# Kernel tuning notes

Measured on AMD Instinct MI355X. Metric: run time of the kernel, lower is better.

## Reference

```python
import jax, jax.numpy as jnp
import numpy as np
from jax import lax
import math

D_MODEL = 768
EXPAND = 2
D_INNER = EXPAND * D_MODEL          # 1536 (= d_ssm since d_ssm=None)
D_STATE = 128
HEADDIM = 64
NHEADS = D_INNER // HEADDIM         # 24
D_CONV = 4
NGROUPS = 1
CONV_DIM = D_INNER + 2 * NGROUPS * D_STATE            # 1792
D_IN_PROJ = 2 * D_INNER + 2 * NGROUPS * D_STATE + NHEADS  # d_mlp = 0
BATCH, SEQLEN = 2, 2048
EPS = 1e-5


def setup_inputs() -> dict:
    key = jax.random.key(0)
    ks = jax.random.split(key, 8)
    u = jax.random.normal(ks[0], (BATCH, SEQLEN, D_MODEL), dtype=jnp.float32)
    in_proj_w = jax.random.normal(ks[1], (D_IN_PROJ, D_MODEL), dtype=jnp.float32) / math.sqrt(D_MODEL)
    conv_w = jax.random.uniform(ks[2], (CONV_DIM, D_CONV), dtype=jnp.float32, minval=-0.5, maxval=0.5)
    conv_b = jnp.zeros((CONV_DIM,), dtype=jnp.float32)
    # dt_bias = inverse-softplus of dt sampled log-uniform in [1e-3, 1e-1]
    dt = jnp.exp(jax.random.uniform(ks[3], (NHEADS,)) * (math.log(0.1) - math.log(0.001)) + math.log(0.001))
    dt_bias = dt + jnp.log(-jnp.expm1(-dt))
    A_log = jnp.log(jax.random.uniform(ks[4], (NHEADS,), minval=1.0, maxval=16.0))
    D = jnp.ones((NHEADS,), dtype=jnp.float32)
    norm_w = jnp.ones((D_INNER,), dtype=jnp.float32)
    out_proj_w = jax.random.normal(ks[5], (D_MODEL, D_INNER), dtype=jnp.float32) / math.sqrt(D_INNER)
    return {"u": u, "in_proj_w": in_proj_w, "conv_w": conv_w, "conv_b": conv_b,
            "dt_bias": dt_bias, "A_log": A_log, "D": D, "norm_w": norm_w,
            "out_proj_w": out_proj_w}


def _mamba2_forward(u, in_proj_w, conv_w, conv_b, dt_bias, A_log, D, norm_w, out_proj_w):
    b, l, _ = u.shape
    zxbcdt = u @ in_proj_w.T                                   # [b,l,D_IN_PROJ]
    z = zxbcdt[..., :D_INNER]                                  # [b,l,d_ssm]
    xBC = zxbcdt[..., D_INNER:D_INNER + CONV_DIM]              # [b,l,conv_dim]
    dt = zxbcdt[..., D_INNER + CONV_DIM:]                      # [b,l,h]

    # causal depthwise conv1d (pad d_conv-1 left == torch pad both + truncate tail)
    xBC_t = xBC.transpose(0, 2, 1)                             # [b,c,l]
    conv_out = lax.conv_general_dilated(
        xBC_t, conv_w[:, None, :], window_strides=(1,),
        padding=[(D_CONV - 1, 0)], feature_group_count=CONV_DIM,
        dimension_numbers=("NCH", "OIH", "NCH"))
    xBC = jax.nn.silu(conv_out + conv_b[None, :, None]).transpose(0, 2, 1)  # [b,l,c]

    x = xBC[..., :D_INNER].reshape(b, l, NHEADS, HEADDIM)      # [b,l,h,p]
    B = xBC[..., D_INNER:D_INNER + D_STATE]                    # [b,l,n]
    C = xBC[..., D_INNER + D_STATE:]                           # [b,l,n]

    A = -jnp.exp(A_log)                                        # [h]
    dt_dis = jax.nn.softplus(dt + dt_bias)                     # [b,l,h]  (dt_limit=(0,inf) -> no-op clamp)
    dA = jnp.exp(dt_dis * A)                                   # [b,l,h]

    def step(state, inp):
        dA_t, dt_t, B_t, x_t, C_t = inp
        dBx = jnp.einsum("bh,bn,bhp->bhpn", dt_t, B_t, x_t)    # [b,h,p,n]
        state = lax.stop_gradient(state * dA_t[:, :, None, None] + dBx)  # matches torch .detach()
        y_t = jnp.einsum("bhpn,bn->bhp", state, C_t)
        return state, y_t

    xs = (dA.transpose(1, 0, 2), dt_dis.transpose(1, 0, 2),
          B.transpose(1, 0, 2), x.transpose(1, 0, 2, 3), C.transpose(1, 0, 2))
    state0 = jnp.zeros((b, NHEADS, HEADDIM, D_STATE), dtype=u.dtype)
    _, ys = lax.scan(step, state0, xs)                         # [l,b,h,p]
    y = ys.transpose(1, 0, 2, 3) + x * D[None, None, :, None]  # D skip (per-head)
    y = y.reshape(b, l, D_INNER)

    # gated RMSNorm (norm_before_gate=False, group_size = d_ssm)
    yz = y * jax.nn.silu(z)
    y = yz * lax.rsqrt(jnp.mean(yz * yz, axis=-1, keepdims=True) + EPS) * norm_w

    return y @ out_proj_w.T                                    # [b,l,d_model]


def reference(u, in_proj_w, conv_w, conv_b, dt_bias, A_log, D, norm_w, out_proj_w):
    return _mamba2_forward(u, in_proj_w, conv_w, conv_b, dt_bias, A_log, D, norm_w, out_proj_w)
```

## Files before the change

kernel.cpp:

```cpp
#include <hip/hip_runtime.h>
#include <hip/hip_bf16.h>
#include <math.h>

#define D_MODEL   768
#define D_INNER   1536
#define D_STATE   128
#define HEADDIM   64
#define NHEADS    24
#define D_CONV    4
#define CONV_DIM  1792
#define D_IN_PROJ 3352
#define BATCH     2
#define SEQLEN    2048
#define NROWS     (BATCH*SEQLEN)
#define EPS       1e-5f

#define NCHUNK    16
#define CHUNK     128
#define STATE_SZ  (HEADDIM*D_STATE)

#define N1_PAD    3456
#define LDST      136
#define H72       72

typedef __bf16 bf16x8 __attribute__((ext_vector_type(8)));
typedef float  f32x4  __attribute__((ext_vector_type(4)));

__device__ __forceinline__ short f2b(float f) {
    unsigned u = __float_as_uint(f);
    unsigned r = (u + 0x7FFFu + ((u >> 16) & 1u)) >> 16;
    return (short)r;
}

__global__ __launch_bounds__(256) void gemm_bf16_kernel(
    const short* __restrict__ A, const short* __restrict__ W,
    float* __restrict__ C, int K, int Nreal)
{
    __shared__ short As[128][32];
    __shared__ short Bs[128][32];
    const int m0 = blockIdx.y * 128;
    const int n0 = blockIdx.x * 128;
    const int tid  = threadIdx.x;
    const int lane = tid & 63;
    const int wid  = tid >> 6;
    const int wm = wid >> 1, wn = wid & 1;
    const int lr = lane & 15;
    const int kg = lane >> 4;

    f32x4 acc[4][4];
    #pragma unroll
    for (int i = 0; i < 4; ++i)
        #pragma unroll
        for (int j = 0; j < 4; ++j)
            acc[i][j] = (f32x4){0.f, 0.f, 0.f, 0.f};

    const int srow = (lane >> 2);
    const int scol = (lane & 3) * 8;

    for (int k0 = 0; k0 < K; k0 += 32) {
        #pragma unroll
        for (int it = 0; it < 2; ++it) {
            int r = wid * 32 + it * 16 + srow;
            const short* ga = A + (size_t)(m0 + r) * K + k0 + scol;
            const short* gw = W + (size_t)(n0 + r) * K + k0 + scol;
            __builtin_amdgcn_global_load_lds(
                (const __attribute__((address_space(1))) void*)ga,
                (__attribute__((address_space(3))) void*)&As[wid * 32 + it * 16][0],
                16, 0, 0);
            __builtin_amdgcn_global_load_lds(
                (const __attribute__((address_space(1))) void*)gw,
                (__attribute__((address_space(3))) void*)&Bs[wid * 32 + it * 16][0],
                16, 0, 0);
        }
        __syncthreads();

        bf16x8 af[4], bf[4];
        #pragma unroll
        for (int i = 0; i < 4; ++i)
            af[i] = *(const bf16x8*)&As[wm * 64 + i * 16 + lr][kg * 8];
        #pragma unroll
        for (int j = 0; j < 4; ++j)
            bf[j] = *(const bf16x8*)&Bs[wn * 64 + j * 16 + lr][kg * 8];
        #pragma unroll
        for (int i = 0; i < 4; ++i)
            #pragma unroll
            for (int j = 0; j < 4; ++j)
                acc[i][j] = __builtin_amdgcn_mfma_f32_16x16x32_bf16(af[i], bf[j], acc[i][j], 0, 0, 0);
        __syncthreads();
    }

    #pragma unroll
    for (int i = 0; i < 4; ++i) {
        int mrow = m0 + wm * 64 + i * 16 + kg * 4;
        #pragma unroll
        for (int j = 0; j < 4; ++j) {
            int ncol = n0 + wn * 64 + j * 16 + lr;
            if (ncol < Nreal) {
                #pragma unroll
                for (int r = 0; r < 4; ++r)
                    C[(size_t)(mrow + r) * Nreal + ncol] = acc[i][j][r];
            }
        }
    }
}

__global__ __launch_bounds__(256) void cast_bf16_kernel(
    const float* __restrict__ in, short* __restrict__ out, int n4)
{
    int i = blockIdx.x * 256 + threadIdx.x;
    if (i >= n4) return;
    float4 v = *(const float4*)(in + (size_t)i * 4);
    short4 o = make_short4(f2b(v.x), f2b(v.y), f2b(v.z), f2b(v.w));
    *(short4*)(out + (size_t)i * 4) = o;
}

__global__ __launch_bounds__(256) void cast_pad_w1_kernel(
    const float* __restrict__ w, short* __restrict__ wb)
{
    int i = blockIdx.x * 256 + threadIdx.x;
    const int n4 = N1_PAD * D_MODEL / 4;
    if (i >= n4) return;
    size_t base = (size_t)i * 4;
    int row = (int)(base / D_MODEL);
    float4 v = make_float4(0.f, 0.f, 0.f, 0.f);
    if (row < D_IN_PROJ) v = *(const float4*)(w + base);
    short4 o = make_short4(f2b(v.x), f2b(v.y), f2b(v.z), f2b(v.w));
    *(short4*)(wb + base) = o;
}

__global__ __launch_bounds__(256) void conv_silu_kernel(
    const float* __restrict__ zx, float* __restrict__ out,
    const float* __restrict__ cw, const float* __restrict__ cb)
{
    int c = blockIdx.x * 256 + threadIdx.x;
    int r = blockIdx.y;
    if (c >= CONV_DIM) return;
    int l = r & (SEQLEN - 1);
    const float4 w = *(const float4*)(cw + (size_t)c * 4);
    const float wj[4] = {w.x, w.y, w.z, w.w};
    const float* col = zx + D_INNER + c;
    float acc = cb[c];
    #pragma unroll
    for (int j = 0; j < 4; ++j) {
        int ll = l - 3 + j;
        if (ll >= 0) acc = fmaf(col[(size_t)(r - 3 + j) * D_IN_PROJ], wj[j], acc);
    }
    out[(size_t)r * CONV_DIM + c] = acc / (1.f + expf(-acc));
}

__global__ __launch_bounds__(256) void dt_kernel(
    const float* __restrict__ zx, const float* __restrict__ dt_bias,
    const float* __restrict__ A_log, float* __restrict__ dtb, float* __restrict__ dta)
{
    int idx = blockIdx.x * 256 + threadIdx.x;
    if (idx >= NROWS * NHEADS) return;
    int r = idx / NHEADS, h = idx - r * NHEADS;
    float x = zx[(size_t)r * D_IN_PROJ + (D_INNER + CONV_DIM) + h] + dt_bias[h];
    float sp = (x > 20.f) ? x : log1pf(expf(x));
    float A  = -expf(A_log[h]);
    dtb[idx] = sp;
    dta[idx] = sp * A;
}

__global__ __launch_bounds__(512) void ssd_intra(
    const float* __restrict__ co, const float* __restrict__ dtb,
    const float* __restrict__ dta, const float* __restrict__ Dvec,
    float* __restrict__ ybuf, float* __restrict__ sstate, float* __restrict__ cumW)
{
    __shared__ short lds[26112];
    __shared__ float clg[128];
    __shared__ float dts[128];

    int t = blockIdx.x;
    int c = t & 15;
    int hb = t >> 4;
    int h = hb % NHEADS;
    int b = hb / NHEADS;
    const int R0 = b * SEQLEN + c * CHUNK;
    const int tid  = threadIdx.x;
    const int lane = tid & 63;
    const int wid  = tid >> 6;
    const int lr = lane & 15;
    const int kg = lane >> 4;
    const float* cobase = co + (size_t)R0 * CONV_DIM;

    if (tid < 128) {
        clg[tid] = dta[(size_t)(R0 + tid) * NHEADS + h];
        dts[tid] = dtb[(size_t)(R0 + tid) * NHEADS + h];
    }
    __syncthreads();
    for (int off = 1; off < 128; off <<= 1) {
        float v = 0.f;
        if (tid < 128 && tid >= off) v = clg[tid - off];
        __syncthreads();
        if (tid < 128) clg[tid] += v;
        __syncthreads();
    }
    const float clgE = clg[127];
    if (tid < 128)
        cumW[((size_t)(b * NHEADS + h)) * SEQLEN + c * CHUNK + tid] = __expf(clg[tid]);

    short* CsH = lds;
    short* BsH = lds + 128 * H72;
    const int wmS = wid >> 2, wnS = wid & 3;
    f32x4 accS[4][2];
    #pragma unroll
    for (int i = 0; i < 4; ++i)
        #pragma unroll
        for (int j = 0; j < 2; ++j)
            accS[i][j] = (f32x4){0.f, 0.f, 0.f, 0.f};

    for (int kh = 0; kh < 2; ++kh) {
        {
            int r = tid >> 2, q = tid & 3;
            const float* cr = cobase + (size_t)r * CONV_DIM + (D_INNER + D_STATE) + kh * 64 + q * 16;
            const float* br = cobase + (size_t)r * CONV_DIM + D_INNER + kh * 64 + q * 16;
            #pragma unroll
            for (int i = 0; i < 4; ++i) {
                float4 cv = *(const float4*)(cr + i * 4);
                float4 bv = *(const float4*)(br + i * 4);
                *(short4*)(CsH + r * H72 + q * 16 + i * 4) =
                    make_short4(f2b(cv.x), f2b(cv.y), f2b(cv.z), f2b(cv.w));
                *(short4*)(BsH + r * H72 + q * 16 + i * 4) =
                    make_short4(f2b(bv.x), f2b(bv.y), f2b(bv.z), f2b(bv.w));
            }
        }
        __syncthreads();
        #pragma unroll
        for (int kk = 0; kk < 2; ++kk) {
            bf16x8 af[4], bf[2];
            #pragma unroll
            for (int i = 0; i < 4; ++i)
                af[i] = *(const bf16x8*)(CsH + (wmS * 64 + i * 16 + lr) * H72 + kk * 32 + kg * 8);
            #pragma unroll
            for (int j = 0; j < 2; ++j)
                bf[j] = *(const bf16x8*)(BsH + (wnS * 32 + j * 16 + lr) * H72 + kk * 32 + kg * 8);
            #pragma unroll
            for (int i = 0; i < 4; ++i)
                #pragma unroll
                for (int j = 0; j < 2; ++j)
                    accS[i][j] = __builtin_amdgcn_mfma_f32_16x16x32_bf16(af[i], bf[j], accS[i][j], 0, 0, 0);
        }
        __syncthreads();
    }

    short* Ps = lds;
    short* Xt = lds + 128 * LDST;
    #pragma unroll
    for (int i = 0; i < 4; ++i) {
        #pragma unroll
        for (int j = 0; j < 2; ++j) {
            #pragma unroll
            for (int r = 0; r < 4; ++r) {
                int l  = wmS * 64 + i * 16 + kg * 4 + r;
                int lp = wnS * 32 + j * 16 + lr;
                float w = (lp <= l) ? __expf(clg[l] - clg[lp]) : 0.f;
                Ps[l * LDST + lp] = f2b(accS[i][j][r] * w);
            }
        }
    }
    if (tid < 256) {
        int r = tid >> 1, q = tid & 1;
        const float* xr = cobase + (size_t)r * CONV_DIM + h * HEADDIM + q * 32;
        float dtv = dts[r];
        #pragma unroll
        for (int i = 0; i < 8; ++i) {
            float4 xv = *(const float4*)(xr + i * 4);
            int p = q * 32 + i * 4;
            Xt[(p + 0) * LDST + r] = f2b(xv.x * dtv);
            Xt[(p + 1) * LDST + r] = f2b(xv.y * dtv);
            Xt[(p + 2) * LDST + r] = f2b(xv.z * dtv);
            Xt[(p + 3) * LDST + r] = f2b(xv.w * dtv);
        }
    }
    __syncthreads();

    {
        int wm = wid >> 1, wn = wid & 1;
        f32x4 acc[2][2];
        #pragma unroll
        for (int i = 0; i < 2; ++i)
            #pragma unroll
            for (int j = 0; j < 2; ++j)
                acc[i][j] = (f32x4){0.f, 0.f, 0.f, 0.f};
        #pragma unroll
        for (int kk = 0; kk < 4; ++kk) {
            bf16x8 af[2], bf[2];
            #pragma unroll
            for (int i = 0; i < 2; ++i)
                af[i] = *(const bf16x8*)(Ps + (wm * 32 + i * 16 + lr) * LDST + kk * 32 + kg * 8);
            #pragma unroll
            for (int j = 0; j < 2; ++j)
                bf[j] = *(const bf16x8*)(Xt + (wn * 32 + j * 16 + lr) * LDST + kk * 32 + kg * 8);
            #pragma unroll
            for (int i = 0; i < 2; ++i)
                #pragma unroll
                for (int j = 0; j < 2; ++j)
                    acc[i][j] = __builtin_amdgcn_mfma_f32_16x16x32_bf16(af[i], bf[j], acc[i][j], 0, 0, 0);
        }
        const float Dh = Dvec[h];
        #pragma unroll
        for (int i = 0; i < 2; ++i) {
            #pragma unroll
            for (int j = 0; j < 2; ++j) {
                #pragma unroll
                for (int r = 0; r < 4; ++r) {
                    int l = wm * 32 + i * 16 + kg * 4 + r;
                    int p = wn * 32 + j * 16 + lr;
                    float xval = cobase[(size_t)l * CONV_DIM + h * HEADDIM + p];
                    ybuf[(size_t)(R0 + l) * D_INNER + h * HEADDIM + p] = acc[i][j][r] + Dh * xval;
                }
            }
        }
    }
    __syncthreads();

    short* Bt = lds;
    {
        int r = tid >> 2, q = tid & 3;
        const float* br = cobase + (size_t)r * CONV_DIM + D_INNER + q * 32;
        float wstr = __expf(clgE - clg[r]);
        #pragma unroll
        for (int i = 0; i < 8; ++i) {
            float4 bv = *(const float4*)(br + i * 4);
            int n = q * 32 + i * 4;
            Bt[(n + 0) * LDST + r] = f2b(bv.x * wstr);
            Bt[(n + 1) * LDST + r] = f2b(bv.y * wstr);
            Bt[(n + 2) * LDST + r] = f2b(bv.z * wstr);
            Bt[(n + 3) * LDST + r] = f2b(bv.w * wstr);
        }
    }
    __syncthreads();

    {
        int wm = wid >> 2, wn = wid & 3;
        f32x4 acc[2][2];
        #pragma unroll
        for (int i = 0; i < 2; ++i)
            #pragma unroll
            for (int j = 0; j < 2; ++j)
                acc[i][j] = (f32x4){0.f, 0.f, 0.f, 0.f};
        #pragma unroll
        for (int kk = 0; kk < 4; ++kk) {
            bf16x8 af[2], bf[2];
            #pragma unroll
            for (int i = 0; i < 2; ++i)
                af[i] = *(const bf16x8*)(Xt + (wm * 32 + i * 16 + lr) * LDST + kk * 32 + kg * 8);
            #pragma unroll
            for (int j = 0; j < 2; ++j)
                bf[j] = *(const bf16x8*)(Bt + (wn * 32 + j * 16 + lr) * LDST + kk * 32 + kg * 8);
            #pragma unroll
            for (int i = 0; i < 2; ++i)
                #pragma unroll
                for (int j = 0; j < 2; ++j)
                    acc[i][j] = __builtin_amdgcn_mfma_f32_16x16x32_bf16(af[i], bf[j], acc[i][j], 0, 0, 0);
        }
        float* sbase = sstate + (((size_t)(b * NHEADS + h)) * NCHUNK + c) * STATE_SZ;
        #pragma unroll
        for (int i = 0; i < 2; ++i) {
            #pragma unroll
            for (int j = 0; j < 2; ++j) {
                #pragma unroll
                for (int r = 0; r < 4; ++r) {
                    int p = wm * 32 + i * 16 + kg * 4 + r;
                    int n = wn * 32 + j * 16 + lr;
                    sbase[p * D_STATE + n] = acc[i][j][r];
                }
            }
        }
    }
}

__global__ __launch_bounds__(256) void scan_chunk_prefix(
    const float* __restrict__ cumW, float* __restrict__ sstate)
{
    int bh = blockIdx.x;
    int tid = threadIdx.x;
    float* base = sstate + (size_t)bh * NCHUNK * STATE_SZ;
    const float* cw = cumW + (size_t)bh * SEQLEN;
    float4 run[8];
    #pragma unroll
    for (int k = 0; k < 8; ++k) run[k] = make_float4(0.f, 0.f, 0.f, 0.f);
    for (int c = 0; c < NCHUNK; ++c) {
        float Ac = cw[c * CHUNK + (CHUNK - 1)];
        float* slab = base + (size_t)c * STATE_SZ;
        #pragma unroll
        for (int k = 0; k < 8; ++k) {
            float* ptr = slab + tid * 4 + k * 1024;
            float4 loc = *(float4*)ptr;
            float4 r = run[k];
            *(float4*)ptr = r;
            run[k].x = fmaf(Ac, r.x, loc.x);
            run[k].y = fmaf(Ac, r.y, loc.y);
            run[k].z = fmaf(Ac, r.z, loc.z);
            run[k].w = fmaf(Ac, r.w, loc.w);
        }
    }
}

__global__ __launch_bounds__(256) void ssd_inter(
    const float* __restrict__ co, const float* __restrict__ cumW,
    const float* __restrict__ sstate, float* __restrict__ ybuf)
{
    __shared__ short lds[26112];
    short* Cs = lds;
    short* Sn = lds + 128 * LDST;

    int t = blockIdx.x;
    int c = t & 15;
    int hb = t >> 4;
    int h = hb % NHEADS;
    int b = hb / NHEADS;
    const int R0 = b * SEQLEN + c * CHUNK;
    const int tid  = threadIdx.x;
    const int lane = tid & 63;
    const int wid  = tid >> 6;
    const int lr = lane & 15;
    const int kg = lane >> 4;
    const float* cobase = co + (size_t)R0 * CONV_DIM;

    {
        int r = tid >> 1, q = tid & 1;
        const float* cr = cobase + (size_t)r * CONV_DIM + (D_INNER + D_STATE) + q * 64;
        #pragma unroll
        for (int i = 0; i < 16; ++i) {
            float4 cv = *(const float4*)(cr + i * 4);
            *(short4*)(Cs + r * LDST + q * 64 + i * 4) =
                make_short4(f2b(cv.x), f2b(cv.y), f2b(cv.z), f2b(cv.w));
        }
    }
    {
        int r = tid >> 2, q = tid & 3;
        const float* sr = sstate + (((size_t)(b * NHEADS + h)) * NCHUNK + c) * STATE_SZ
                          + (size_t)r * D_STATE + q * 32;
        #pragma unroll
        for (int i = 0; i < 8; ++i) {
            float4 sv = *(const float4*)(sr + i * 4);
            *(short4*)(Sn + r * LDST + q * 32 + i * 4) =
                make_short4(f2b(sv.x), f2b(sv.y), f2b(sv.z), f2b(sv.w));
        }
    }
    __syncthreads();

    int wm = wid >> 1, wn = wid & 1;
    f32x4 acc[4][2];
    #pragma unroll
    for (int i = 0; i < 4; ++i)
        #pragma unroll
        for (int j = 0; j < 2; ++j)
            acc[i][j] = (f32x4){0.f, 0.f, 0.f, 0.f};
    #pragma unroll
    for (int kk = 0; kk < 4; ++kk) {
        bf16x8 af[4], bf[2];
        #pragma unroll
        for (int i = 0; i < 4; ++i)
            af[i] = *(const bf16x8*)(Cs + (wm * 64 + i * 16 + lr) * LDST + kk * 32 + kg * 8);
        #pragma unroll
        for (int j = 0; j < 2; ++j)
            bf[j] = *(const bf16x8*)(Sn + (wn * 32 + j * 16 + lr) * LDST + kk * 32 + kg * 8);
        #pragma unroll
        for (int i = 0; i < 4; ++i)
            #pragma unroll
            for (int j = 0; j < 2; ++j)
                acc[i][j] = __builtin_amdgcn_mfma_f32_16x16x32_bf16(af[i], bf[j], acc[i][j], 0, 0, 0);
    }
    const float* cwrow = cumW + ((size_t)(b * NHEADS + h)) * SEQLEN + c * CHUNK;
    #pragma unroll
    for (int i = 0; i < 4; ++i) {
        #pragma unroll
        for (int j = 0; j < 2; ++j) {
            #pragma unroll
            for (int r = 0; r < 4; ++r) {
                int l = wm * 64 + i * 16 + kg * 4 + r;
                int p = wn * 32 + j * 16 + lr;
                float w = cwrow[l];
                size_t idx = (size_t)(R0 + l) * D_INNER + h * HEADDIM + p;
                ybuf[idx] += w * acc[i][j][r];
            }
        }
    }
}

__global__ __launch_bounds__(256) void gate_norm_kernel(
    const float* __restrict__ zx, const float* __restrict__ ybuf,
    const float* __restrict__ norm_w, short* __restrict__ yn)
{
    int r = blockIdx.x;
    const float* zrow = zx + (size_t)r * D_IN_PROJ;
    const float* yrow = ybuf + (size_t)r * D_INNER;
    float vals[6];
    float ss = 0.f;
    #pragma unroll
    for (int i = 0; i < 6; ++i) {
        int c = threadIdx.x + i * 256;
        float z = zrow[c];
        float y = yrow[c];
        float v = y * (z / (1.f + expf(-z)));
        vals[i] = v;
        ss = fmaf(v, v, ss);
    }
    ss += __shfl_xor(ss, 1);
    ss += __shfl_xor(ss, 2);
    ss += __shfl_xor(ss, 4);
    ss += __shfl_xor(ss, 8);
    ss += __shfl_xor(ss, 16);
    ss += __shfl_xor(ss, 32);
    __shared__ float red[4];
    if ((threadIdx.x & 63) == 0) red[threadIdx.x >> 6] = ss;
    __syncthreads();
    float tot = red[0] + red[1] + red[2] + red[3];
    float scale = rsqrtf(tot / (float)D_INNER + EPS);
    #pragma unroll
    for (int i = 0; i < 6; ++i) {
        int c = threadIdx.x + i * 256;
        yn[(size_t)r * D_INNER + c] = f2b(vals[i] * scale * norm_w[c]);
    }
}

extern "C" void kernel_launch(void* const* d_in, const int* in_sizes, int n_in,
                              void* d_out, int out_size, void* d_ws, size_t ws_size,
                              hipStream_t stream) {
    const float* u          = (const float*)d_in[0];
    const float* in_proj_w  = (const float*)d_in[1];
    const float* conv_w     = (const float*)d_in[2];
    const float* conv_b     = (const float*)d_in[3];
    const float* dt_bias    = (const float*)d_in[4];
    const float* A_log      = (const float*)d_in[5];
    const float* Dvec       = (const float*)d_in[6];
    const float* norm_w     = (const float*)d_in[7];
    const float* out_proj_w = (const float*)d_in[8];
    float* out = (float*)d_out;

    float* zx     = (float*)d_ws;
    float* co     = zx     + (size_t)NROWS * D_IN_PROJ;
    float* dtb    = co     + (size_t)NROWS * CONV_DIM;
    float* dta    = dtb    + (size_t)NROWS * NHEADS;
    float* ybuf   = dta    + (size_t)NROWS * NHEADS;
    float* sstate = ybuf   + (size_t)NROWS * D_INNER;
    float* cumW   = sstate + (size_t)BATCH*NHEADS*NCHUNK*STATE_SZ;

    short* ub  = (short*)ybuf;
    short* w1b = (short*)(ybuf + (size_t)NROWS * D_MODEL/2);
    short* ynb = (short*)co;
    short* w2b = (short*)zx;

    cast_bf16_kernel<<<(NROWS*D_MODEL/4 + 255)/256, 256, 0, stream>>>(u, ub, NROWS*D_MODEL/4);
    cast_pad_w1_kernel<<<(N1_PAD*D_MODEL/4 + 255)/256, 256, 0, stream>>>(in_proj_w, w1b);
    gemm_bf16_kernel<<<dim3(N1_PAD/128, NROWS/128), 256, 0, stream>>>(ub, w1b, zx, D_MODEL, D_IN_PROJ);
    conv_silu_kernel<<<dim3(CONV_DIM/256, NROWS), 256, 0, stream>>>(zx, co, conv_w, conv_b);
    dt_kernel<<<(NROWS*NHEADS + 255)/256, 256, 0, stream>>>(zx, dt_bias, A_log, dtb, dta);
    ssd_intra<<<BATCH*NHEADS*NCHUNK, 512, 0, stream>>>(co, dtb, dta, Dvec, ybuf, sstate, cumW);
    scan_chunk_prefix<<<BATCH*NHEADS, 256, 0, stream>>>(cumW, sstate);
    ssd_inter<<<BATCH*NHEADS*NCHUNK, 256, 0, stream>>>(co, cumW, sstate, ybuf);
    gate_norm_kernel<<<NROWS, 256, 0, stream>>>(zx, ybuf, norm_w, ynb);
    cast_bf16_kernel<<<(D_MODEL*D_INNER/4 + 255)/256, 256, 0, stream>>>(out_proj_w, w2b, D_MODEL*D_INNER/4);
    gemm_bf16_kernel<<<dim3(D_MODEL/128, NROWS/128), 256, 0, stream>>>(ynb, w2b, out, D_INNER, D_MODEL);
}
```

Before: 292.6 us.

## Store in_proj and conv outputs as bf16 and parallelize chunk prefix scan

The first GEMM now writes its output in bf16, and the conv kernel reads bf16 and writes bf16. It processes 8 channels per thread with vector loads. The SSD kernels, dt, and gate_norm consume these bf16 buffers directly, which halves intermediate memory traffic and removes the casts they used to do themselves. The chunk prefix scan is split across 16 times more blocks, so the serial chunk loop runs with more parallelism. This adds bf16 rounding on z, dt and conv outputs and reshuffles workspace aliasing.

```diff
diff --git a/kernel.cpp b/kernel.cpp
--- a/kernel.cpp
+++ b/kernel.cpp
@@ -25,16 +25,21 @@
 
 typedef __bf16 bf16x8 __attribute__((ext_vector_type(8)));
 typedef float  f32x4  __attribute__((ext_vector_type(4)));
+typedef short  s16x8  __attribute__((ext_vector_type(8)));
 
 __device__ __forceinline__ short f2b(float f) {
     unsigned u = __float_as_uint(f);
     unsigned r = (u + 0x7FFFu + ((u >> 16) & 1u)) >> 16;
     return (short)r;
 }
-
+__device__ __forceinline__ float b2f(short s) {
+    return __uint_as_float(((unsigned)(unsigned short)s) << 16);
+}
+
+template<typename OT>
 __global__ __launch_bounds__(256) void gemm_bf16_kernel(
     const short* __restrict__ A, const short* __restrict__ W,
-    float* __restrict__ C, int K, int Nreal)
+    OT* __restrict__ C, int K, int Nreal)
 {
     __shared__ short As[128][32];
     __shared__ short Bs[128][32];
@@ -97,8 +102,12 @@
             int ncol = n0 + wn * 64 + j * 16 + lr;
             if (ncol < Nreal) {
                 #pragma unroll
-                for (int r = 0; r < 4; ++r)
-                    C[(size_t)(mrow + r) * Nreal + ncol] = acc[i][j][r];
+                for (int r = 0; r < 4; ++r) {
+                    if constexpr (sizeof(OT) == 2)
+                        C[(size_t)(mrow + r) * Nreal + ncol] = f2b(acc[i][j][r]);
+                    else
+                        C[(size_t)(mrow + r) * Nreal + ncol] = acc[i][j][r];
+                }
             }
         }
     }
@@ -129,33 +138,53 @@
 }
 
 __global__ __launch_bounds__(256) void conv_silu_kernel(
-    const float* __restrict__ zx, float* __restrict__ out,
+    const short* __restrict__ zxb, short* __restrict__ cob,
     const float* __restrict__ cw, const float* __restrict__ cb)
 {
-    int c = blockIdx.x * 256 + threadIdx.x;
-    int r = blockIdx.y;
-    if (c >= CONV_DIM) return;
+    const int NG = CONV_DIM / 8;
+    int idx = blockIdx.x * 256 + threadIdx.x;
+    int g = idx % NG;
+    int r = idx / NG;
+    int c0 = g * 8;
     int l = r & (SEQLEN - 1);
-    const float4 w = *(const float4*)(cw + (size_t)c * 4);
-    const float wj[4] = {w.x, w.y, w.z, w.w};
-    const float* col = zx + D_INNER + c;
-    float acc = cb[c];
-    #pragma unroll
-    for (int j = 0; j < 4; ++j) {
-        int ll = l - 3 + j;
-        if (ll >= 0) acc = fmaf(col[(size_t)(r - 3 + j) * D_IN_PROJ], wj[j], acc);
-    }
-    out[(size_t)r * CONV_DIM + c] = acc / (1.f + expf(-acc));
+
+    float4 w[8];
+    #pragma unroll
+    for (int e = 0; e < 8; ++e)
+        w[e] = *(const float4*)(cw + (size_t)(c0 + e) * 4);
+
+    float acc[8];
+    #pragma unroll
+    for (int e = 0; e < 8; ++e) acc[e] = cb[c0 + e];
+
+    #pragma unroll
+    for (int tap = 0; tap < 4; ++tap) {
+        if (l - 3 + tap >= 0) {
+            s16x8 v = *(const s16x8*)(zxb + (size_t)(r - 3 + tap) * D_IN_PROJ + D_INNER + c0);
+            const float wt[4] = {0, 0, 0, 0};
+            #pragma unroll
+            for (int e = 0; e < 8; ++e) {
+                float we = (tap == 0) ? w[e].x : (tap == 1) ? w[e].y : (tap == 2) ? w[e].z : w[e].w;
+                acc[e] = fmaf(b2f(v[e]), we, acc[e]);
+            }
+            (void)wt;
+        }
+    }
+    s16x8 o;
+    #pragma unroll
+    for (int e = 0; e < 8; ++e)
+        o[e] = f2b(acc[e] / (1.f + expf(-acc[e])));
+    *(s16x8*)(cob + (size_t)r * CONV_DIM + c0) = o;
 }
 
 __global__ __launch_bounds__(256) void dt_kernel(
-    const float* __restrict__ zx, const float* __restrict__ dt_bias,
+    const short* __restrict__ zxb, const float* __restrict__ dt_bias,
     const float* __restrict__ A_log, float* __restrict__ dtb, float* __restrict__ dta)
 {
     int idx = blockIdx.x * 256 + threadIdx.x;
     if (idx >= NROWS * NHEADS) return;
     int r = idx / NHEADS, h = idx - r * NHEADS;
-    float x = zx[(size_t)r * D_IN_PROJ + (D_INNER + CONV_DIM) + h] + dt_bias[h];
+    float x = b2f(zxb[(size_t)r * D_IN_PROJ + (D_INNER + CONV_DIM) + h]) + dt_bias[h];
     float sp = (x > 20.f) ? x : log1pf(expf(x));
     float A  = -expf(A_log[h]);
     dtb[idx] = sp;
@@ -163,7 +192,7 @@
 }
 
 __global__ __launch_bounds__(512) void ssd_intra(
-    const float* __restrict__ co, const float* __restrict__ dtb,
+    const short* __restrict__ co, const float* __restrict__ dtb,
     const float* __restrict__ dta, const float* __restrict__ Dvec,
     float* __restrict__ ybuf, float* __restrict__ sstate, float* __restrict__ cumW)
 {
@@ -182,7 +211,7 @@
     const int wid  = tid >> 6;
     const int lr = lane & 15;
     const int kg = lane >> 4;
-    const float* cobase = co + (size_t)R0 * CONV_DIM;
+    const short* cobase = co + (size_t)R0 * CONV_DIM;
 
     if (tid < 128) {
         clg[tid] = dta[(size_t)(R0 + tid) * NHEADS + h];
@@ -213,17 +242,12 @@
     for (int kh = 0; kh < 2; ++kh) {
         {
             int r = tid >> 2, q = tid & 3;
-            const float* cr = cobase + (size_t)r * CONV_DIM + (D_INNER + D_STATE) + kh * 64 + q * 16;
-            const float* br = cobase + (size_t)r * CONV_DIM + D_INNER + kh * 64 + q * 16;
-            #pragma unroll
-            for (int i = 0; i < 4; ++i) {
-                float4 cv = *(const float4*)(cr + i * 4);
-                float4 bv = *(const float4*)(br + i * 4);
-                *(short4*)(CsH + r * H72 + q * 16 + i * 4) =
-                    make_short4(f2b(cv.x), f2b(cv.y), f2b(cv.z), f2b(cv.w));
-                *(short4*)(BsH + r * H72 + q * 16 + i * 4) =
-                    make_short4(f2b(bv.x), f2b(bv.y), f2b(bv.z), f2b(bv.w));
-            }
+            const short* cr = cobase + (size_t)r * CONV_DIM + (D_INNER + D_STATE) + kh * 64 + q * 16;
+            const short* br = cobase + (size_t)r * CONV_DIM + D_INNER + kh * 64 + q * 16;
+            *(s16x8*)(CsH + r * H72 + q * 16)     = *(const s16x8*)cr;
+            *(s16x8*)(CsH + r * H72 + q * 16 + 8) = *(const s16x8*)(cr + 8);
+            *(s16x8*)(BsH + r * H72 + q * 16)     = *(const s16x8*)br;
+            *(s16x8*)(BsH + r * H72 + q * 16 + 8) = *(const s16x8*)(br + 8);
         }
         __syncthreads();
         #pragma unroll
@@ -261,16 +285,16 @@
     }
     if (tid < 256) {
         int r = tid >> 1, q = tid & 1;
-        const float* xr = cobase + (size_t)r * CONV_DIM + h * HEADDIM + q * 32;
+        const short* xr = cobase + (size_t)r * CONV_DIM + h * HEADDIM + q * 32;
         float dtv = dts[r];
         #pragma unroll
-        for (int i = 0; i < 8; ++i) {
-            float4 xv = *(const float4*)(xr + i * 4);
-            int p = q * 32 + i * 4;
-            Xt[(p + 0) * LDST + r] = f2b(xv.x * dtv);
-            Xt[(p + 1) * LDST + r] = f2b(xv.y * dtv);
-            Xt[(p + 2) * LDST + r] = f2b(xv.z * dtv);
-            Xt[(p + 3) * LDST + r] = f2b(xv.w * dtv);
+        for (int i = 0; i < 4; ++i) {
+            s16x8 xv = *(const s16x8*)(xr + i * 8);
+            #pragma unroll
+            for (int e = 0; e < 8; ++e) {
+                int p = q * 32 + i * 8 + e;
+                Xt[p * LDST + r] = f2b(b2f(xv[e]) * dtv);
+            }
         }
     }
     __syncthreads();
@@ -307,7 +331,7 @@
                 for (int r = 0; r < 4; ++r) {
                     int l = wm * 32 + i * 16 + kg * 4 + r;
                     int p = wn * 32 + j * 16 + lr;
-                    float xval = cobase[(size_t)l * CONV_DIM + h * HEADDIM + p];
+                    float xval = b2f(cobase[(size_t)l * CONV_DIM + h * HEADDIM + p]);
                     ybuf[(size_t)(R0 + l) * D_INNER + h * HEADDIM + p] = acc[i][j][r] + Dh * xval;
                 }
             }
@@ -318,16 +342,16 @@
     short* Bt = lds;
     {
         int r = tid >> 2, q = tid & 3;
-        const float* br = cobase + (size_t)r * CONV_DIM + D_INNER + q * 32;
+        const short* br = cobase + (size_t)r * CONV_DIM + D_INNER + q * 32;
         float wstr = __expf(clgE - clg[r]);
         #pragma unroll
-        for (int i = 0; i < 8; ++i) {
-            float4 bv = *(const float4*)(br + i * 4);
-            int n = q * 32 + i * 4;
-            Bt[(n + 0) * LDST + r] = f2b(bv.x * wstr);
-            Bt[(n + 1) * LDST + r] = f2b(bv.y * wstr);
-            Bt[(n + 2) * LDST + r] = f2b(bv.z * wstr);
-            Bt[(n + 3) * LDST + r] = f2b(bv.w * wstr);
+        for (int i = 0; i < 4; ++i) {
+            s16x8 bv = *(const s16x8*)(br + i * 8);
+            #pragma unroll
+            for (int e = 0; e < 8; ++e) {
+                int n = q * 32 + i * 8 + e;
+                Bt[n * LDST + r] = f2b(b2f(bv[e]) * wstr);
+            }
         }
     }
     __syncthreads();
@@ -371,35 +395,30 @@
     }
 }
 
-__global__ __launch_bounds__(256) void scan_chunk_prefix(
+__global__ __launch_bounds__(128) void scan_chunk_prefix(
     const float* __restrict__ cumW, float* __restrict__ sstate)
 {
-    int bh = blockIdx.x;
+    int blk = blockIdx.x;
+    int piece = blk & 15;
+    int bh = blk >> 4;
     int tid = threadIdx.x;
-    float* base = sstate + (size_t)bh * NCHUNK * STATE_SZ;
+    float* base = sstate + (size_t)bh * NCHUNK * STATE_SZ + piece * 512 + tid * 4;
     const float* cw = cumW + (size_t)bh * SEQLEN;
-    float4 run[8];
-    #pragma unroll
-    for (int k = 0; k < 8; ++k) run[k] = make_float4(0.f, 0.f, 0.f, 0.f);
+    float4 run = make_float4(0.f, 0.f, 0.f, 0.f);
     for (int c = 0; c < NCHUNK; ++c) {
         float Ac = cw[c * CHUNK + (CHUNK - 1)];
-        float* slab = base + (size_t)c * STATE_SZ;
-        #pragma unroll
-        for (int k = 0; k < 8; ++k) {
-            float* ptr = slab + tid * 4 + k * 1024;
-            float4 loc = *(float4*)ptr;
-            float4 r = run[k];
-            *(float4*)ptr = r;
-            run[k].x = fmaf(Ac, r.x, loc.x);
-            run[k].y = fmaf(Ac, r.y, loc.y);
-            run[k].z = fmaf(Ac, r.z, loc.z);
-            run[k].w = fmaf(Ac, r.w, loc.w);
-        }
+        float* ptr = base + (size_t)c * STATE_SZ;
+        float4 loc = *(float4*)ptr;
+        *(float4*)ptr = run;
+        run.x = fmaf(Ac, run.x, loc.x);
+        run.y = fmaf(Ac, run.y, loc.y);
+        run.z = fmaf(Ac, run.z, loc.z);
+        run.w = fmaf(Ac, run.w, loc.w);
     }
 }
 
 __global__ __launch_bounds__(256) void ssd_inter(
-    const float* __restrict__ co, const float* __restrict__ cumW,
+    const short* __restrict__ co, const float* __restrict__ cumW,
     const float* __restrict__ sstate, float* __restrict__ ybuf)
 {
     __shared__ short lds[26112];
@@ -417,17 +436,14 @@
     const int wid  = tid >> 6;
     const int lr = lane & 15;
     const int kg = lane >> 4;
-    const float* cobase = co + (size_t)R0 * CONV_DIM;
+    const short* cobase = co + (size_t)R0 * CONV_DIM;
 
     {
         int r = tid >> 1, q = tid & 1;
-        const float* cr = cobase + (size_t)r * CONV_DIM + (D_INNER + D_STATE) + q * 64;
-        #pragma unroll
-        for (int i = 0; i < 16; ++i) {
-            float4 cv = *(const float4*)(cr + i * 4);
-            *(short4*)(Cs + r * LDST + q * 64 + i * 4) =
-                make_short4(f2b(cv.x), f2b(cv.y), f2b(cv.z), f2b(cv.w));
-        }
+        const short* cr = cobase + (size_t)r * CONV_DIM + (D_INNER + D_STATE) + q * 64;
+        #pragma unroll
+        for (int i = 0; i < 8; ++i)
+            *(s16x8*)(Cs + r * LDST + q * 64 + i * 8) = *(const s16x8*)(cr + i * 8);
     }
     {
         int r = tid >> 2, q = tid & 3;
@@ -482,18 +498,18 @@
 }
 
 __global__ __launch_bounds__(256) void gate_norm_kernel(
-    const float* __restrict__ zx, const float* __restrict__ ybuf,
+    const short* __restrict__ zxb, const float* __restrict__ ybuf,
     const float* __restrict__ norm_w, short* __restrict__ yn)
 {
     int r = blockIdx.x;
-    const float* zrow = zx + (size_t)r * D_IN_PROJ;
+    const short* zrow = zxb + (size_t)r * D_IN_PROJ;
     const float* yrow = ybuf + (size_t)r * D_INNER;
     float vals[6];
     float ss = 0.f;
     #pragma unroll
     for (int i = 0; i < 6; ++i) {
         int c = threadIdx.x + i * 256;
-        float z = zrow[c];
+        float z = b2f(zrow[c]);
         float y = yrow[c];
         float v = y * (z / (1.f + expf(-z)));
         vals[i] = v;
@@ -531,28 +547,28 @@
     const float* out_proj_w = (const float*)d_in[8];
     float* out = (float*)d_out;
 
-    float* zx     = (float*)d_ws;
-    float* co     = zx     + (size_t)NROWS * D_IN_PROJ;
-    float* dtb    = co     + (size_t)NROWS * CONV_DIM;
-    float* dta    = dtb    + (size_t)NROWS * NHEADS;
-    float* ybuf   = dta    + (size_t)NROWS * NHEADS;
-    float* sstate = ybuf   + (size_t)NROWS * D_INNER;
+    short* zxb    = (short*)d_ws;
+    short* cob    = zxb + (size_t)NROWS * D_IN_PROJ;
+    float* dtb    = (float*)(cob + (size_t)NROWS * CONV_DIM);
+    float* dta    = dtb  + (size_t)NROWS * NHEADS;
+    float* ybuf   = dta  + (size_t)NROWS * NHEADS;
+    float* sstate = ybuf + (size_t)NROWS * D_INNER;
     float* cumW   = sstate + (size_t)BATCH*NHEADS*NCHUNK*STATE_SZ;
 
     short* ub  = (short*)ybuf;
-    short* w1b = (short*)(ybuf + (size_t)NROWS * D_MODEL/2);
-    short* ynb = (short*)co;
-    short* w2b = (short*)zx;
+    short* w1b = ub + (size_t)NROWS * D_MODEL;
+    short* ynb = (short*)sstate;
+    short* w2b = zxb;
 
     cast_bf16_kernel<<<(NROWS*D_MODEL/4 + 255)/256, 256, 0, stream>>>(u, ub, NROWS*D_MODEL/4);
     cast_pad_w1_kernel<<<(N1_PAD*D_MODEL/4 + 255)/256, 256, 0, stream>>>(in_proj_w, w1b);
-    gemm_bf16_kernel<<<dim3(N1_PAD/128, NROWS/128), 256, 0, stream>>>(ub, w1b, zx, D_MODEL, D_IN_PROJ);
-    conv_silu_kernel<<<dim3(CONV_DIM/256, NROWS), 256, 0, stream>>>(zx, co, conv_w, conv_b);
-    dt_kernel<<<(NROWS*NHEADS + 255)/256, 256, 0, stream>>>(zx, dt_bias, A_log, dtb, dta);
-    ssd_intra<<<BATCH*NHEADS*NCHUNK, 512, 0, stream>>>(co, dtb, dta, Dvec, ybuf, sstate, cumW);
-    scan_chunk_prefix<<<BATCH*NHEADS, 256, 0, stream>>>(cumW, sstate);
-    ssd_inter<<<BATCH*NHEADS*NCHUNK, 256, 0, stream>>>(co, cumW, sstate, ybuf);
-    gate_norm_kernel<<<NROWS, 256, 0, stream>>>(zx, ybuf, norm_w, ynb);
+    gemm_bf16_kernel<short><<<dim3(N1_PAD/128, NROWS/128), 256, 0, stream>>>(ub, w1b, zxb, D_MODEL, D_IN_PROJ);
+    conv_silu_kernel<<<NROWS*(CONV_DIM/8)/256, 256, 0, stream>>>(zxb, cob, conv_w, conv_b);
+    dt_kernel<<<(NROWS*NHEADS + 255)/256, 256, 0, stream>>>(zxb, dt_bias, A_log, dtb, dta);
+    ssd_intra<<<BATCH*NHEADS*NCHUNK, 512, 0, stream>>>(cob, dtb, dta, Dvec, ybuf, sstate, cumW);
+    scan_chunk_prefix<<<BATCH*NHEADS*16, 128, 0, stream>>>(cumW, sstate);
+    ssd_inter<<<BATCH*NHEADS*NCHUNK, 256, 0, stream>>>(cob, cumW, sstate, ybuf);
+    gate_norm_kernel<<<NROWS, 256, 0, stream>>>(zxb, ybuf, norm_w, ynb);
     cast_bf16_kernel<<<(D_MODEL*D_INNER/4 + 255)/256, 256, 0, stream>>>(out_proj_w, w2b, D_MODEL*D_INNER/4);
-    gemm_bf16_kernel<<<dim3(D_MODEL/128, NROWS/128), 256, 0, stream>>>(ynb, w2b, out, D_INNER, D_MODEL);
-}
+    gemm_bf16_kernel<float><<<dim3(D_MODEL/128, NROWS/128), 256, 0, stream>>>(ynb, w2b, out, D_INNER, D_MODEL);
+}
```

Measured after the change: 262.8 us. -10.2%, faster.
